# Performance work log

Measured on AMD Instinct MI355X. Metric: run time of the kernel, lower is better.

The kernel has to match this reference:

```python
import jax, jax.numpy as jnp
import numpy as np

B, Q, K, D = 32, 1024, 1024, 64
MASK_VAL = -1000000.0  # matches torch source's -1e6 fill


def setup_inputs() -> dict:
    key = jax.random.key(0)
    kq, kk, kv, kl = jax.random.split(key, 4)
    return {
        "queries": jax.random.normal(kq, (B, Q, D), dtype=jnp.float32),
        "keys": jax.random.normal(kk, (B, K, D), dtype=jnp.float32),
        "values": jax.random.normal(kv, (B, K, D), dtype=jnp.float32),
        "valid_lens": jax.random.randint(kl, (B,), 1, K + 1, dtype=jnp.int64),
    }


def reference(queries, keys, values, valid_lens):
    d = queries.shape[-1]
    # [B, Q, K] scores
    scores = jnp.einsum("bqd,bkd->bqk", queries, keys) / jnp.sqrt(jnp.asarray(d, queries.dtype))
    # 1D valid_lens -> same length mask for every query row of a batch element
    kv_pos = jnp.arange(scores.shape[-1])  # [K]
    mask = kv_pos[None, None, :] < valid_lens[:, None, None]  # [B, 1, K] broadcast
    scores = jnp.where(mask, scores, MASK_VAL)
    attn = jax.nn.softmax(scores, axis=-1)
    # dropout p=0.0 -> identity
    return jnp.einsum("bqk,bkd->bqd", attn, values)
```

## Files before the change

### kernel.cpp

```cpp
#include <hip/hip_runtime.h>
#include <hip/hip_bf16.h>

#define NB 32
#define NQ 1024
#define NK 1024
#define ND 64
#define BK 64
#define M_FIX 16.0f

typedef __attribute__((ext_vector_type(8))) __bf16 bf16x8;
typedef __attribute__((ext_vector_type(8))) short  s16x8;
typedef __attribute__((ext_vector_type(4))) float  f32x4;

static __device__ __forceinline__ short f2bf(float f) {
  unsigned u = __builtin_bit_cast(unsigned, f);
  u += 0x7fffu + ((u >> 16) & 1u);
  return (short)(u >> 16);
}

static __device__ __forceinline__ int swzoff(int row, int gcol) {
  return row * 64 + (((gcol ^ (row & 7)) & 7) << 3);
}

#define GLD_LDS16(gp, lp)                                              \
  __builtin_amdgcn_global_load_lds(                                    \
      (const __attribute__((address_space(1))) void*)(gp),             \
      (__attribute__((address_space(3))) void*)(lp), 16, 0, 0)

__launch_bounds__(256)
__global__ void prep_kv(const float* __restrict__ Kp, const float* __restrict__ Vp,
                        const int* __restrict__ VLp,
                        short* __restrict__ Kb, short* __restrict__ Vt) {
  __shared__ __align__(16) short T[64 * 72];
  const int wg = blockIdx.x;
  const int b  = wg >> 4;
  const int kt = wg & 15;

  const bool is64 = (VLp[1] == 0);
  const int  len  = is64 ? VLp[2 * b] : VLp[b];
  if (kt * 64 >= len) return;

  const int tid = threadIdx.x;

  {
    const int key = tid >> 2, d0 = (tid & 3) * 16, g0 = (tid & 3) * 2;
    const float* src = Kp + ((size_t)(b * NK + kt * 64 + key)) * ND + d0;
    short out[16];
#pragma unroll
    for (int i = 0; i < 16; i += 4) {
      float4 v = *(const float4*)(src + i);
      out[i] = f2bf(v.x); out[i + 1] = f2bf(v.y);
      out[i + 2] = f2bf(v.z); out[i + 3] = f2bf(v.w);
    }
    short* dtile = Kb + ((size_t)(b * 16 + kt)) * 4096;
    *(s16x8*)&dtile[swzoff(key, g0)]     = *(const s16x8*)out;
    *(s16x8*)&dtile[swzoff(key, g0 + 1)] = *(const s16x8*)(out + 8);
  }

  {
    const int vkey = tid & 63, vd0 = (tid >> 6) * 16;
    const float* src = Vp + ((size_t)(b * NK + kt * 64 + vkey)) * ND + vd0;
#pragma unroll
    for (int i = 0; i < 4; ++i) {
      float4 v = *(const float4*)(src + i * 4);
      T[(vd0 + i * 4 + 0) * 72 + vkey] = f2bf(v.x);
      T[(vd0 + i * 4 + 1) * 72 + vkey] = f2bf(v.y);
      T[(vd0 + i * 4 + 2) * 72 + vkey] = f2bf(v.z);
      T[(vd0 + i * 4 + 3) * 72 + vkey] = f2bf(v.w);
    }
  }
  __syncthreads();
  {
    const int d = tid >> 2, c = (tid & 3) * 16, g0 = (tid & 3) * 2;
    short* vtile = Vt + ((size_t)(b * 16 + kt)) * 4096;
    *(s16x8*)&vtile[swzoff(d, g0)]     = *(const s16x8*)&T[d * 72 + c];
    *(s16x8*)&vtile[swzoff(d, g0 + 1)] = *(const s16x8*)&T[d * 72 + c + 8];
  }
}

__launch_bounds__(512, 4)
__global__ void attn_fwd(const float* __restrict__ Qp,
                         const short* __restrict__ Kb,
                         const short* __restrict__ Vt,
                         const int* __restrict__ VLp,
                         float* __restrict__ Op) {
  __shared__ __align__(16) short SM[40960];

  const int wg  = blockIdx.x;
  const int swz = (wg & 7) * 64 + (wg >> 3);
  const int b   = swz >> 4;
  const int qb  = swz & 15;

  const int tid  = threadIdx.x;
  const int wid  = tid >> 6;
  const int lane = tid & 63;
  const int l16  = lane & 15;
  const int grp  = lane >> 4;
  const int qgrp = wid >> 1;
  const int par  = wid & 1;

  const bool is64 = (VLp[1] == 0);
  const int  len  = is64 ? VLp[2 * b] : VLp[b];
  const int  ntiles = (len + BK - 1) >> 6;
  const int  nsup   = (ntiles + 1) >> 1;

  const float qscale = 0.125f * 1.44269504088896341f;

  bf16x8 qf[2];
  {
    const float* qsrc = Qp + ((size_t)(b * NQ + qb * 64 + qgrp * 16 + l16)) * ND + grp * 8;
#pragma unroll
    for (int ks = 0; ks < 2; ++ks) {
      float4 a = *(const float4*)(qsrc + ks * 32);
      float4 c = *(const float4*)(qsrc + ks * 32 + 4);
      s16x8 t;
      t[0] = f2bf(a.x * qscale); t[1] = f2bf(a.y * qscale);
      t[2] = f2bf(a.z * qscale); t[3] = f2bf(a.w * qscale);
      t[4] = f2bf(c.x * qscale); t[5] = f2bf(c.y * qscale);
      t[6] = f2bf(c.z * qscale); t[7] = f2bf(c.w * qscale);
      qf[ks] = __builtin_bit_cast(bf16x8, t);
    }
  }

  const short* kg = Kb + (size_t)b * 16 * 4096;
  const short* vg = Vt + (size_t)b * 16 * 4096;

  auto dma = [&](int buf, int t0) {
    GLD_LDS16(kg + (size_t)t0 * 4096 + tid * 8,       &SM[buf * 8192 + wid * 512]);
    GLD_LDS16(kg + (size_t)(t0 + 1) * 4096 + tid * 8, &SM[buf * 8192 + 4096 + wid * 512]);
    GLD_LDS16(vg + (size_t)t0 * 4096 + tid * 8,       &SM[16384 + buf * 8192 + wid * 512]);
    GLD_LDS16(vg + (size_t)(t0 + 1) * 4096 + tid * 8, &SM[16384 + buf * 8192 + 4096 + wid * 512]);
  };

  const f32x4 vzero = {0.f, 0.f, 0.f, 0.f};
  f32x4 oacc[4];
#pragma unroll
  for (int i = 0; i < 4; ++i) oacc[i] = vzero;
  float lrun[4] = {0.f, 0.f, 0.f, 0.f};

  short* pw = &SM[32768 + wid * 1024];

  dma(0, 0);
  int buf = 0;

  for (int it = 0; it < nsup; ++it) {
    if (it + 1 < nsup) {
      dma(buf ^ 1, 2 * (it + 1));
      asm volatile("s_waitcnt vmcnt(4)" ::: "memory");
    } else {
      asm volatile("s_waitcnt vmcnt(0)" ::: "memory");
    }
    __builtin_amdgcn_sched_barrier(0);
    __builtin_amdgcn_s_barrier();
    __builtin_amdgcn_sched_barrier(0);

    const int myt = 2 * it + par;
    if (myt < ntiles) {
      const short* kw = &SM[buf * 8192 + par * 4096];
      const short* vw = &SM[16384 + buf * 8192 + par * 4096];

      f32x4 sc[4];
      __builtin_amdgcn_s_setprio(1);
#pragma unroll
      for (int n = 0; n < 4; ++n) {
        f32x4 acc = vzero;
#pragma unroll
        for (int ks = 0; ks < 2; ++ks) {
          bf16x8 kf = __builtin_bit_cast(bf16x8,
              *(const s16x8*)&kw[swzoff(n * 16 + l16, ks * 4 + grp)]);
          acc = __builtin_amdgcn_mfma_f32_16x16x32_bf16(qf[ks], kf, acc, 0, 0, 0);
        }
        sc[n] = acc;
      }
      __builtin_amdgcn_s_setprio(0);

#pragma unroll
      for (int n = 0; n < 4; ++n) {
        const bool ok = (myt * BK + n * 16 + l16) < len;
#pragma unroll
        for (int r = 0; r < 4; ++r) {
          float pv = ok ? exp2f(sc[n][r] - M_FIX) : 0.0f;
          sc[n][r] = pv;
          lrun[r] += pv;
        }
      }

#pragma unroll
      for (int n = 0; n < 4; ++n)
#pragma unroll
        for (int r = 0; r < 4; ++r) {
          const int row = grp * 4 + r;
          const int gc  = n * 2 + (l16 >> 3);
          pw[row * 64 + ((((gc ^ (row & 7)) & 7)) << 3) + (l16 & 7)] = f2bf(sc[n][r]);
        }

      asm volatile("s_waitcnt lgkmcnt(0)" ::: "memory");
      __builtin_amdgcn_sched_barrier(0);

      bf16x8 pf[2];
#pragma unroll
      for (int ks = 0; ks < 2; ++ks)
        pf[ks] = __builtin_bit_cast(bf16x8,
            *(const s16x8*)&pw[swzoff(l16, ks * 4 + grp)]);

      __builtin_amdgcn_s_setprio(1);
#pragma unroll
      for (int nd = 0; nd < 4; ++nd) {
#pragma unroll
        for (int ks = 0; ks < 2; ++ks) {
          bf16x8 vf = __builtin_bit_cast(bf16x8,
              *(const s16x8*)&vw[swzoff(nd * 16 + l16, ks * 4 + grp)]);
          oacc[nd] = __builtin_amdgcn_mfma_f32_16x16x32_bf16(pf[ks], vf, oacc[nd], 0, 0, 0);
        }
      }
      __builtin_amdgcn_s_setprio(0);
    }

    asm volatile("s_waitcnt lgkmcnt(0)" ::: "memory");
    __builtin_amdgcn_sched_barrier(0);
    __builtin_amdgcn_s_barrier();
    __builtin_amdgcn_sched_barrier(0);
    buf ^= 1;
  }

  __syncthreads();
  float* CB = (float*)SM;
  const int crow = qgrp * 64 + lane;
  if (par == 1) {
    float* dst = CB + (size_t)crow * 20;
#pragma unroll
    for (int nd = 0; nd < 4; ++nd) *(f32x4*)(dst + nd * 4) = oacc[nd];
    f32x4 lv = {lrun[0], lrun[1], lrun[2], lrun[3]};
    *(f32x4*)(dst + 16) = lv;
  }
  __syncthreads();
  if (par == 0) {
    const float* src = CB + (size_t)crow * 20;
#pragma unroll
    for (int nd = 0; nd < 4; ++nd) oacc[nd] += *(const f32x4*)(src + nd * 4);
    f32x4 lv = *(const f32x4*)(src + 16);
    float inv[4];
#pragma unroll
    for (int r = 0; r < 4; ++r) {
      float l = lrun[r] + lv[r];
#pragma unroll
      for (int off = 1; off < 16; off <<= 1)
        l += __shfl_xor(l, off);
      inv[r] = 1.0f / l;
    }
    float* obase = Op + ((size_t)(b * NQ + qb * 64 + qgrp * 16)) * ND;
#pragma unroll
    for (int nd = 0; nd < 4; ++nd)
#pragma unroll
      for (int r = 0; r < 4; ++r)
        obase[(grp * 4 + r) * ND + nd * 16 + l16] = oacc[nd][r] * inv[r];
  }
}

extern "C" void kernel_launch(void* const* d_in, const int* in_sizes, int n_in,
                              void* d_out, int out_size, void* d_ws, size_t ws_size,
                              hipStream_t stream) {
  const float* Qp = (const float*)d_in[0];
  const float* Kp = (const float*)d_in[1];
  const float* Vp = (const float*)d_in[2];
  const int*   VL = (const int*)d_in[3];
  float* Op = (float*)d_out;

  short* Kb = (short*)d_ws;
  short* Vt = Kb + (size_t)NB * NK * ND;

  prep_kv<<<dim3(NB * 16), dim3(256), 0, stream>>>(Kp, Vp, VL, Kb, Vt);
  attn_fwd<<<dim3(NB * 16), dim3(512), 0, stream>>>(Qp, Kb, Vt, VL, Op);
}
```

Measured before the change: 33.09 us.

## Split key range across two workgroups per query tile with atomic-flag reduction

Launches twice as many attention workgroups, each covering half of the valid key tiles for a (batch, query-block) pair. The first finisher writes its partial output and row sums to a workspace and sets a flag, and the second waits on the flag, combines the partials, normalizes and writes the final output. Counters and flags are reset in the prep kernel. This aims to fill the GPU better, since 512 workgroups underuse the compute units. The cost is extra workspace traffic, a spin-wait that relies on the partner workgroup being resident, and some duplicated Q loading.

```diff
diff --git a/kernel.cpp b/kernel.cpp
--- a/kernel.cpp
+++ b/kernel.cpp
@@ -6,6 +6,7 @@
 #define NK 1024
 #define ND 64
 #define BK 64
+#define NPAIR (NB * 16)
 #define M_FIX 16.0f
 
 typedef __attribute__((ext_vector_type(8))) __bf16 bf16x8;
@@ -30,11 +31,14 @@
 __launch_bounds__(256)
 __global__ void prep_kv(const float* __restrict__ Kp, const float* __restrict__ Vp,
                         const int* __restrict__ VLp,
-                        short* __restrict__ Kb, short* __restrict__ Vt) {
+                        short* __restrict__ Kb, short* __restrict__ Vt,
+                        int* __restrict__ Cnt, int* __restrict__ Flg) {
   __shared__ __align__(16) short T[64 * 72];
   const int wg = blockIdx.x;
   const int b  = wg >> 4;
   const int kt = wg & 15;
+
+  if (threadIdx.x == 0) { Cnt[wg] = 0; Flg[wg] = 0; }
 
   const bool is64 = (VLp[1] == 0);
   const int  len  = is64 ? VLp[2 * b] : VLp[b];
@@ -83,13 +87,18 @@
                          const short* __restrict__ Kb,
                          const short* __restrict__ Vt,
                          const int* __restrict__ VLp,
+                         float* __restrict__ Po, float* __restrict__ Pl,
+                         int* __restrict__ Cnt, int* __restrict__ Flg,
                          float* __restrict__ Op) {
   __shared__ __align__(16) short SM[40960];
-
-  const int wg  = blockIdx.x;
-  const int swz = (wg & 7) * 64 + (wg >> 3);
-  const int b   = swz >> 4;
-  const int qb  = swz & 15;
+  __shared__ int roleSh;
+
+  const int wg   = blockIdx.x;
+  const int pair = wg & (NPAIR - 1);
+  const int ks   = wg >> 9;
+  const int swz  = (pair & 7) * 64 + (pair >> 3);
+  const int b    = swz >> 4;
+  const int qb   = swz & 15;
 
   const int tid  = threadIdx.x;
   const int wid  = tid >> 6;
@@ -102,7 +111,10 @@
   const bool is64 = (VLp[1] == 0);
   const int  len  = is64 ? VLp[2 * b] : VLp[b];
   const int  ntiles = (len + BK - 1) >> 6;
-  const int  nsup   = (ntiles + 1) >> 1;
+  const int  half   = (ntiles + 1) >> 1;
+  const int  lo     = ks ? half : 0;
+  const int  hi     = ks ? ntiles : half;
+  const int  ns     = (hi - lo + 1) >> 1;
 
   const float qscale = 0.125f * 1.44269504088896341f;
 
@@ -110,15 +122,15 @@
   {
     const float* qsrc = Qp + ((size_t)(b * NQ + qb * 64 + qgrp * 16 + l16)) * ND + grp * 8;
 #pragma unroll
-    for (int ks = 0; ks < 2; ++ks) {
-      float4 a = *(const float4*)(qsrc + ks * 32);
-      float4 c = *(const float4*)(qsrc + ks * 32 + 4);
+    for (int k2 = 0; k2 < 2; ++k2) {
+      float4 a = *(const float4*)(qsrc + k2 * 32);
+      float4 c = *(const float4*)(qsrc + k2 * 32 + 4);
       s16x8 t;
       t[0] = f2bf(a.x * qscale); t[1] = f2bf(a.y * qscale);
       t[2] = f2bf(a.z * qscale); t[3] = f2bf(a.w * qscale);
       t[4] = f2bf(c.x * qscale); t[5] = f2bf(c.y * qscale);
       t[6] = f2bf(c.z * qscale); t[7] = f2bf(c.w * qscale);
-      qf[ks] = __builtin_bit_cast(bf16x8, t);
+      qf[k2] = __builtin_bit_cast(bf16x8, t);
     }
   }
 
@@ -140,12 +152,12 @@
 
   short* pw = &SM[32768 + wid * 1024];
 
-  dma(0, 0);
+  if (ns > 0) dma(0, lo);
   int buf = 0;
 
-  for (int it = 0; it < nsup; ++it) {
-    if (it + 1 < nsup) {
-      dma(buf ^ 1, 2 * (it + 1));
+  for (int it = 0; it < ns; ++it) {
+    if (it + 1 < ns) {
+      dma(buf ^ 1, lo + 2 * (it + 1));
       asm volatile("s_waitcnt vmcnt(4)" ::: "memory");
     } else {
       asm volatile("s_waitcnt vmcnt(0)" ::: "memory");
@@ -154,8 +166,8 @@
     __builtin_amdgcn_s_barrier();
     __builtin_amdgcn_sched_barrier(0);
 
-    const int myt = 2 * it + par;
-    if (myt < ntiles) {
+    const int myt = lo + 2 * it + par;
+    if (myt < hi) {
       const short* kw = &SM[buf * 8192 + par * 4096];
       const short* vw = &SM[16384 + buf * 8192 + par * 4096];
 
@@ -165,10 +177,10 @@
       for (int n = 0; n < 4; ++n) {
         f32x4 acc = vzero;
 #pragma unroll
-        for (int ks = 0; ks < 2; ++ks) {
+        for (int k2 = 0; k2 < 2; ++k2) {
           bf16x8 kf = __builtin_bit_cast(bf16x8,
-              *(const s16x8*)&kw[swzoff(n * 16 + l16, ks * 4 + grp)]);
-          acc = __builtin_amdgcn_mfma_f32_16x16x32_bf16(qf[ks], kf, acc, 0, 0, 0);
+              *(const s16x8*)&kw[swzoff(n * 16 + l16, k2 * 4 + grp)]);
+          acc = __builtin_amdgcn_mfma_f32_16x16x32_bf16(qf[k2], kf, acc, 0, 0, 0);
         }
         sc[n] = acc;
       }
@@ -199,18 +211,18 @@
 
       bf16x8 pf[2];
 #pragma unroll
-      for (int ks = 0; ks < 2; ++ks)
-        pf[ks] = __builtin_bit_cast(bf16x8,
-            *(const s16x8*)&pw[swzoff(l16, ks * 4 + grp)]);
+      for (int k2 = 0; k2 < 2; ++k2)
+        pf[k2] = __builtin_bit_cast(bf16x8,
+            *(const s16x8*)&pw[swzoff(l16, k2 * 4 + grp)]);
 
       __builtin_amdgcn_s_setprio(1);
 #pragma unroll
       for (int nd = 0; nd < 4; ++nd) {
 #pragma unroll
-        for (int ks = 0; ks < 2; ++ks) {
+        for (int k2 = 0; k2 < 2; ++k2) {
           bf16x8 vf = __builtin_bit_cast(bf16x8,
-              *(const s16x8*)&vw[swzoff(nd * 16 + l16, ks * 4 + grp)]);
-          oacc[nd] = __builtin_amdgcn_mfma_f32_16x16x32_bf16(pf[ks], vf, oacc[nd], 0, 0, 0);
+              *(const s16x8*)&vw[swzoff(nd * 16 + l16, k2 * 4 + grp)]);
+          oacc[nd] = __builtin_amdgcn_mfma_f32_16x16x32_bf16(pf[k2], vf, oacc[nd], 0, 0, 0);
         }
       }
       __builtin_amdgcn_s_setprio(0);
@@ -234,26 +246,68 @@
     *(f32x4*)(dst + 16) = lv;
   }
   __syncthreads();
+  float lsum[4] = {0.f, 0.f, 0.f, 0.f};
   if (par == 0) {
     const float* src = CB + (size_t)crow * 20;
 #pragma unroll
     for (int nd = 0; nd < 4; ++nd) oacc[nd] += *(const f32x4*)(src + nd * 4);
     f32x4 lv = *(const f32x4*)(src + 16);
-    float inv[4];
 #pragma unroll
     for (int r = 0; r < 4; ++r) {
       float l = lrun[r] + lv[r];
 #pragma unroll
       for (int off = 1; off < 16; off <<= 1)
         l += __shfl_xor(l, off);
-      inv[r] = 1.0f / l;
-    }
-    float* obase = Op + ((size_t)(b * NQ + qb * 64 + qgrp * 16)) * ND;
-#pragma unroll
-    for (int nd = 0; nd < 4; ++nd)
+      lsum[r] = l;
+    }
+  }
+
+  if (tid == 0) roleSh = atomicAdd(&Cnt[pair], 1);
+  __syncthreads();
+  const int role = roleSh;
+
+  float* Po_ = Po + (size_t)pair * 4096;
+  float* Pl_ = Pl + (size_t)pair * 64;
+
+  if (role == 0) {
+    if (par == 0) {
+#pragma unroll
+      for (int nd = 0; nd < 4; ++nd)
+#pragma unroll
+        for (int r = 0; r < 4; ++r)
+          Po_[(qgrp * 16 + grp * 4 + r) * 64 + nd * 16 + l16] = oacc[nd][r];
+      if (l16 == 0) {
+#pragma unroll
+        for (int r = 0; r < 4; ++r)
+          Pl_[qgrp * 16 + grp * 4 + r] = lsum[r];
+      }
+    }
+    __syncthreads();
+    if (tid == 0)
+      __hip_atomic_store(&Flg[pair], 1, __ATOMIC_RELEASE, __HIP_MEMORY_SCOPE_AGENT);
+  } else {
+    if (tid == 0) {
+      while (!__hip_atomic_load(&Flg[pair], __ATOMIC_ACQUIRE, __HIP_MEMORY_SCOPE_AGENT))
+        __builtin_amdgcn_s_sleep(8);
+    }
+    __syncthreads();
+    if (par == 0) {
+#pragma unroll
+      for (int nd = 0; nd < 4; ++nd)
+#pragma unroll
+        for (int r = 0; r < 4; ++r)
+          oacc[nd][r] += Po_[(qgrp * 16 + grp * 4 + r) * 64 + nd * 16 + l16];
+      float inv[4];
 #pragma unroll
       for (int r = 0; r < 4; ++r)
-        obase[(grp * 4 + r) * ND + nd * 16 + l16] = oacc[nd][r] * inv[r];
+        inv[r] = 1.0f / (lsum[r] + Pl_[qgrp * 16 + grp * 4 + r]);
+      float* obase = Op + ((size_t)(b * NQ + qb * 64 + qgrp * 16)) * ND;
+#pragma unroll
+      for (int nd = 0; nd < 4; ++nd)
+#pragma unroll
+        for (int r = 0; r < 4; ++r)
+          obase[(grp * 4 + r) * ND + nd * 16 + l16] = oacc[nd][r] * inv[r];
+    }
   }
 }
 
@@ -268,7 +322,11 @@
 
   short* Kb = (short*)d_ws;
   short* Vt = Kb + (size_t)NB * NK * ND;
-
-  prep_kv<<<dim3(NB * 16), dim3(256), 0, stream>>>(Kp, Vp, VL, Kb, Vt);
-  attn_fwd<<<dim3(NB * 16), dim3(512), 0, stream>>>(Qp, Kb, Vt, VL, Op);
-}
+  float* Po = (float*)(Vt + (size_t)NB * NK * ND);
+  float* Pl = Po + (size_t)NPAIR * 4096;
+  int*   Cnt = (int*)(Pl + NPAIR * 64);
+  int*   Flg = Cnt + NPAIR;
+
+  prep_kv<<<dim3(NPAIR), dim3(256), 0, stream>>>(Kp, Vp, VL, Kb, Vt, Cnt, Flg);
+  attn_fwd<<<dim3(2 * NPAIR), dim3(512), 0, stream>>>(Qp, Kb, Vt, VL, Po, Pl, Cnt, Flg, Op);
+}
```

After: 62.54 us. 89.0% more time.

## Transpose QK^T MFMA output so each lane holds one query row

Applied to the files above, without the earlier changes.

Swaps the MFMA operand order so the score tile comes out transposed: each lane owns one query row and four keys per fragment. This lets the running row sum be a single scalar, and lets P be written to LDS as packed bf16 pairs via v_cvt_pk_bf16_f32 using precomputed swizzled dword addresses. Masking is limited to the last tile only, and the final normalization needs fewer shuffles. In exchange, P-store addressing and the final row-sum shuffle mapping become more intricate and easier to get wrong.

```diff
diff --git a/kernel.cpp b/kernel.cpp
--- a/kernel.cpp
+++ b/kernel.cpp
@@ -96,6 +96,7 @@
   const int lane = tid & 63;
   const int l16  = lane & 15;
   const int grp  = lane >> 4;
+  const int esw  = l16 & 7;
   const int qgrp = wid >> 1;
   const int par  = wid & 1;
 
@@ -103,6 +104,7 @@
   const int  len  = is64 ? VLp[2 * b] : VLp[b];
   const int  ntiles = (len + BK - 1) >> 6;
   const int  nsup   = (ntiles + 1) >> 1;
+  const int  remLast = len - ((ntiles - 1) << 6);
 
   const float qscale = 0.125f * 1.44269504088896341f;
 
@@ -110,15 +112,15 @@
   {
     const float* qsrc = Qp + ((size_t)(b * NQ + qb * 64 + qgrp * 16 + l16)) * ND + grp * 8;
 #pragma unroll
-    for (int ks = 0; ks < 2; ++ks) {
-      float4 a = *(const float4*)(qsrc + ks * 32);
-      float4 c = *(const float4*)(qsrc + ks * 32 + 4);
+    for (int k2 = 0; k2 < 2; ++k2) {
+      float4 a = *(const float4*)(qsrc + k2 * 32);
+      float4 c = *(const float4*)(qsrc + k2 * 32 + 4);
       s16x8 t;
       t[0] = f2bf(a.x * qscale); t[1] = f2bf(a.y * qscale);
       t[2] = f2bf(a.z * qscale); t[3] = f2bf(a.w * qscale);
       t[4] = f2bf(c.x * qscale); t[5] = f2bf(c.y * qscale);
       t[6] = f2bf(c.z * qscale); t[7] = f2bf(c.w * qscale);
-      qf[ks] = __builtin_bit_cast(bf16x8, t);
+      qf[k2] = __builtin_bit_cast(bf16x8, t);
     }
   }
 
@@ -132,13 +134,24 @@
     GLD_LDS16(vg + (size_t)(t0 + 1) * 4096 + tid * 8, &SM[16384 + buf * 8192 + 4096 + wid * 512]);
   };
 
+  short* pw  = &SM[32768 + wid * 1024];
+  int*   pwd = (int*)pw;
+  int paddr[8];
+#pragma unroll
+  for (int n = 0; n < 4; ++n)
+#pragma unroll
+    for (int a = 0; a < 2; ++a)
+      paddr[n * 2 + a] = l16 * 32 + (((2 * n + (grp >> 1)) ^ esw) << 2) + ((2 * grp + a) & 3);
+  int prd[2];
+#pragma unroll
+  for (int ks = 0; ks < 2; ++ks)
+    prd[ks] = l16 * 64 + (((4 * ks + grp) ^ esw) << 3);
+
   const f32x4 vzero = {0.f, 0.f, 0.f, 0.f};
   f32x4 oacc[4];
 #pragma unroll
   for (int i = 0; i < 4; ++i) oacc[i] = vzero;
-  float lrun[4] = {0.f, 0.f, 0.f, 0.f};
-
-  short* pw = &SM[32768 + wid * 1024];
+  float lrun = 0.f;
 
   dma(0, 0);
   int buf = 0;
@@ -165,33 +178,44 @@
       for (int n = 0; n < 4; ++n) {
         f32x4 acc = vzero;
 #pragma unroll
-        for (int ks = 0; ks < 2; ++ks) {
+        for (int k2 = 0; k2 < 2; ++k2) {
           bf16x8 kf = __builtin_bit_cast(bf16x8,
-              *(const s16x8*)&kw[swzoff(n * 16 + l16, ks * 4 + grp)]);
-          acc = __builtin_amdgcn_mfma_f32_16x16x32_bf16(qf[ks], kf, acc, 0, 0, 0);
+              *(const s16x8*)&kw[swzoff(n * 16 + l16, k2 * 4 + grp)]);
+          acc = __builtin_amdgcn_mfma_f32_16x16x32_bf16(kf, qf[k2], acc, 0, 0, 0);
         }
         sc[n] = acc;
       }
       __builtin_amdgcn_s_setprio(0);
 
-#pragma unroll
-      for (int n = 0; n < 4; ++n) {
-        const bool ok = (myt * BK + n * 16 + l16) < len;
-#pragma unroll
-        for (int r = 0; r < 4; ++r) {
-          float pv = ok ? exp2f(sc[n][r] - M_FIX) : 0.0f;
-          sc[n][r] = pv;
-          lrun[r] += pv;
-        }
+      if (myt == ntiles - 1) {
+#pragma unroll
+        for (int n = 0; n < 4; ++n)
+#pragma unroll
+          for (int r = 0; r < 4; ++r) {
+            float x = (n * 16 + grp * 4 + r < remLast) ? sc[n][r] - M_FIX : -128.0f;
+            float pv = exp2f(x);
+            sc[n][r] = pv;
+            lrun += pv;
+          }
+      } else {
+#pragma unroll
+        for (int n = 0; n < 4; ++n)
+#pragma unroll
+          for (int r = 0; r < 4; ++r) {
+            float pv = exp2f(sc[n][r] - M_FIX);
+            sc[n][r] = pv;
+            lrun += pv;
+          }
       }
 
 #pragma unroll
       for (int n = 0; n < 4; ++n)
 #pragma unroll
-        for (int r = 0; r < 4; ++r) {
-          const int row = grp * 4 + r;
-          const int gc  = n * 2 + (l16 >> 3);
-          pw[row * 64 + ((((gc ^ (row & 7)) & 7)) << 3) + (l16 & 7)] = f2bf(sc[n][r]);
+        for (int a = 0; a < 2; ++a) {
+          int d;
+          asm("v_cvt_pk_bf16_f32 %0, %1, %2"
+              : "=v"(d) : "v"(sc[n][2 * a]), "v"(sc[n][2 * a + 1]));
+          pwd[paddr[n * 2 + a]] = d;
         }
 
       asm volatile("s_waitcnt lgkmcnt(0)" ::: "memory");
@@ -200,17 +224,16 @@
       bf16x8 pf[2];
 #pragma unroll
       for (int ks = 0; ks < 2; ++ks)
-        pf[ks] = __builtin_bit_cast(bf16x8,
-            *(const s16x8*)&pw[swzoff(l16, ks * 4 + grp)]);
+        pf[ks] = __builtin_bit_cast(bf16x8, *(const s16x8*)&pw[prd[ks]]);
 
       __builtin_amdgcn_s_setprio(1);
 #pragma unroll
       for (int nd = 0; nd < 4; ++nd) {
 #pragma unroll
-        for (int ks = 0; ks < 2; ++ks) {
+        for (int k2 = 0; k2 < 2; ++k2) {
           bf16x8 vf = __builtin_bit_cast(bf16x8,
-              *(const s16x8*)&vw[swzoff(nd * 16 + l16, ks * 4 + grp)]);
-          oacc[nd] = __builtin_amdgcn_mfma_f32_16x16x32_bf16(pf[ks], vf, oacc[nd], 0, 0, 0);
+              *(const s16x8*)&vw[swzoff(nd * 16 + l16, k2 * 4 + grp)]);
+          oacc[nd] = __builtin_amdgcn_mfma_f32_16x16x32_bf16(pf[k2], vf, oacc[nd], 0, 0, 0);
         }
       }
       __builtin_amdgcn_s_setprio(0);
@@ -230,30 +253,28 @@
     float* dst = CB + (size_t)crow * 20;
 #pragma unroll
     for (int nd = 0; nd < 4; ++nd) *(f32x4*)(dst + nd * 4) = oacc[nd];
-    f32x4 lv = {lrun[0], lrun[1], lrun[2], lrun[3]};
-    *(f32x4*)(dst + 16) = lv;
+    dst[16] = lrun;
   }
   __syncthreads();
   if (par == 0) {
     const float* src = CB + (size_t)crow * 20;
 #pragma unroll
     for (int nd = 0; nd < 4; ++nd) oacc[nd] += *(const f32x4*)(src + nd * 4);
-    f32x4 lv = *(const f32x4*)(src + 16);
-    float inv[4];
-#pragma unroll
-    for (int r = 0; r < 4; ++r) {
-      float l = lrun[r] + lv[r];
-#pragma unroll
-      for (int off = 1; off < 16; off <<= 1)
-        l += __shfl_xor(l, off);
-      inv[r] = 1.0f / l;
-    }
+    float l = lrun + src[16];
+    l += __shfl_xor(l, 16);
+    l += __shfl_xor(l, 32);
+    const float inv = 1.0f / l;
+    float invr[4];
+#pragma unroll
+    for (int r = 0; r < 4; ++r)
+      invr[r] = __shfl(inv, (lane & 48) | (grp * 4 + r));
+
     float* obase = Op + ((size_t)(b * NQ + qb * 64 + qgrp * 16)) * ND;
 #pragma unroll
     for (int nd = 0; nd < 4; ++nd)
 #pragma unroll
       for (int r = 0; r < 4; ++r)
-        obase[(grp * 4 + r) * ND + nd * 16 + l16] = oacc[nd][r] * inv[r];
+        obase[(grp * 4 + r) * ND + nd * 16 + l16] = oacc[nd][r] * invr[r];
   }
 }
 
```

Measured after the change: 30.57 us. 1.08x faster.
